# Performance work log

Hardware: AMD Instinct MI355X
Metric: run time of the kernel (lower is better)

## Reference

```python
import jax, jax.numpy as jnp
import numpy as np


def setup_inputs() -> dict:
    key = jax.random.key(0)
    x = jax.random.normal(key, (16384, 4096), dtype=jnp.float32)
    return {"x": x}


def reference(x):
    # Row-wise softmax exactly as the torch module: exp(x) / sum(exp(x), axis=-1)
    # (original has no max-subtraction; single exp pass, fused normalize)
    e = jnp.exp(x)
    return e / jnp.sum(e, axis=-1, keepdims=True)
```

## Files before the change

### kernel.cpp

```cpp
#include <hip/hip_runtime.h>


constexpr int COLS = 4096;
constexpr int THREADS = 256;
constexpr int VEC = 4;
constexpr int PER_THREAD = COLS / (THREADS * VEC);

__global__ __launch_bounds__(THREADS) void softmax_rows_kernel(
    const float* __restrict__ x, float* __restrict__ out) {
  const long long row = blockIdx.x;
  const float4* __restrict__ xin =
      reinterpret_cast<const float4*>(x + row * COLS);
  float4* __restrict__ xout = reinterpret_cast<float4*>(out + row * COLS);

  const int tid = threadIdx.x;

  float4 e[PER_THREAD];
  float local = 0.0f;
#pragma unroll
  for (int k = 0; k < PER_THREAD; ++k) {
    float4 v = xin[tid + k * THREADS];
    e[k].x = __expf(v.x);
    e[k].y = __expf(v.y);
    e[k].z = __expf(v.z);
    e[k].w = __expf(v.w);
    local += (e[k].x + e[k].y) + (e[k].z + e[k].w);
  }

#pragma unroll
  for (int off = 32; off > 0; off >>= 1)
    local += __shfl_down(local, off, 64);

  __shared__ float wsum[THREADS / 64];
  const int lane = tid & 63;
  const int wave = tid >> 6;
  if (lane == 0) wsum[wave] = local;
  __syncthreads();

  const float total = (wsum[0] + wsum[1]) + (wsum[2] + wsum[3]);
  const float inv = 1.0f / total;

#pragma unroll
  for (int k = 0; k < PER_THREAD; ++k) {
    float4 o;
    o.x = e[k].x * inv;
    o.y = e[k].y * inv;
    o.z = e[k].z * inv;
    o.w = e[k].w * inv;
    xout[tid + k * THREADS] = o;
  }
}

extern "C" void kernel_launch(void* const* d_in, const int* in_sizes, int n_in,
                              void* d_out, int out_size, void* d_ws,
                              size_t ws_size, hipStream_t stream) {
  const float* x = (const float*)d_in[0];
  float* out = (float*)d_out;
  const int rows = in_sizes[0] / COLS;
  softmax_rows_kernel<<<rows, THREADS, 0, stream>>>(x, out);
}
```

Baseline: 426.6 us.

## Map one row per wavefront and use nontemporal loads and stores

Each 64-lane wavefront now handles a full row, so the row reduction is done with xor shuffles alone and the shared-memory exchange and block barrier are gone. Each lane keeps 16 float4 values (64 floats) in registers, which raises register pressure. The launch bounds ask for 4 blocks per CU to limit that, at some risk to occupancy. Global loads and stores use nontemporal builtins to reduce cache pollution on this purely streaming workload.

```diff
diff --git a/kernel.cpp b/kernel.cpp
--- a/kernel.cpp
+++ b/kernel.cpp
@@ -1,53 +1,46 @@
 #include <hip/hip_runtime.h>
 
 
+typedef float fvec4 __attribute__((ext_vector_type(4)));
+
 constexpr int COLS = 4096;
 constexpr int THREADS = 256;
-constexpr int VEC = 4;
-constexpr int PER_THREAD = COLS / (THREADS * VEC);
+constexpr int WAVES_PER_BLOCK = THREADS / 64;
+constexpr int V4_PER_LANE = COLS / (64 * 4);
 
-__global__ __launch_bounds__(THREADS) void softmax_rows_kernel(
-    const float* __restrict__ x, float* __restrict__ out) {
-  const long long row = blockIdx.x;
-  const float4* __restrict__ xin =
-      reinterpret_cast<const float4*>(x + row * COLS);
-  float4* __restrict__ xout = reinterpret_cast<float4*>(out + row * COLS);
+__global__ __launch_bounds__(THREADS, 4) void softmax_rows_kernel(
+    const float* __restrict__ x, float* __restrict__ out, int rows) {
+  const int wave = threadIdx.x >> 6;
+  const int lane = threadIdx.x & 63;
+  const long long row = (long long)blockIdx.x * WAVES_PER_BLOCK + wave;
+  if (row >= rows) return;
 
-  const int tid = threadIdx.x;
+  const fvec4* __restrict__ xin =
+      reinterpret_cast<const fvec4*>(x + row * COLS);
+  fvec4* __restrict__ xout = reinterpret_cast<fvec4*>(out + row * COLS);
 
-  float4 e[PER_THREAD];
+  fvec4 e[V4_PER_LANE];
   float local = 0.0f;
 #pragma unroll
-  for (int k = 0; k < PER_THREAD; ++k) {
-    float4 v = xin[tid + k * THREADS];
-    e[k].x = __expf(v.x);
-    e[k].y = __expf(v.y);
-    e[k].z = __expf(v.z);
-    e[k].w = __expf(v.w);
-    local += (e[k].x + e[k].y) + (e[k].z + e[k].w);
+  for (int k = 0; k < V4_PER_LANE; ++k) {
+    fvec4 v = __builtin_nontemporal_load(&xin[lane + k * 64]);
+    e[k][0] = __expf(v[0]);
+    e[k][1] = __expf(v[1]);
+    e[k][2] = __expf(v[2]);
+    e[k][3] = __expf(v[3]);
+    local += (e[k][0] + e[k][1]) + (e[k][2] + e[k][3]);
   }
 
 #pragma unroll
   for (int off = 32; off > 0; off >>= 1)
-    local += __shfl_down(local, off, 64);
+    local += __shfl_xor(local, off, 64);
 
-  __shared__ float wsum[THREADS / 64];
-  const int lane = tid & 63;
-  const int wave = tid >> 6;
-  if (lane == 0) wsum[wave] = local;
-  __syncthreads();
-
-  const float total = (wsum[0] + wsum[1]) + (wsum[2] + wsum[3]);
-  const float inv = 1.0f / total;
+  const float inv = 1.0f / local;
 
 #pragma unroll
-  for (int k = 0; k < PER_THREAD; ++k) {
-    float4 o;
-    o.x = e[k].x * inv;
-    o.y = e[k].y * inv;
-    o.z = e[k].z * inv;
-    o.w = e[k].w * inv;
-    xout[tid + k * THREADS] = o;
+  for (int k = 0; k < V4_PER_LANE; ++k) {
+    fvec4 o = e[k] * inv;
+    __builtin_nontemporal_store(o, &xout[lane + k * 64]);
   }
 }
 
@@ -57,5 +50,6 @@
   const float* x = (const float*)d_in[0];
   float* out = (float*)d_out;
   const int rows = in_sizes[0] / COLS;
-  softmax_rows_kernel<<<rows, THREADS, 0, stream>>>(x, out);
+  const int blocks = (rows + WAVES_PER_BLOCK - 1) / WAVES_PER_BLOCK;
+  softmax_rows_kernel<<<blocks, THREADS, 0, stream>>>(x, out, rows);
 }
```

Measured after the change: 419.1 us. No clear change (-1.8%).
